# Optimization experiments

Measured on AMD Instinct MI355X. Metric: run time of the kernel, lower is better.

## Reference

```python
import jax, jax.numpy as jnp
import numpy as np

D_MODEL = 1024
NUM_HEADS = 16
D_FF = 4096
MAX_SEQ_LEN = 2048
THETA = 10000.0
EPS = 1e-5
B, S = 2, 2048


def setup_inputs() -> dict:
    key = jax.random.key(0)
    ks = jax.random.split(key, 10)
    scale = 0.02
    inp = {
        "in_features": jax.random.normal(ks[0], (B, S, D_MODEL), dtype=jnp.float32),
        "token_positions": jnp.broadcast_to(jnp.arange(S, dtype=jnp.int32), (B, S)),
        "q_w": jax.random.normal(ks[1], (D_MODEL, D_MODEL), dtype=jnp.float32) * scale,
        "k_w": jax.random.normal(ks[2], (D_MODEL, D_MODEL), dtype=jnp.float32) * scale,
        "v_w": jax.random.normal(ks[3], (D_MODEL, D_MODEL), dtype=jnp.float32) * scale,
        "o_w": jax.random.normal(ks[4], (D_MODEL, D_MODEL), dtype=jnp.float32) * scale,
        "ln1_w": jnp.ones((D_MODEL,), dtype=jnp.float32),
        "ln2_w": jnp.ones((D_MODEL,), dtype=jnp.float32),
        "ffn_w1": jax.random.normal(ks[5], (D_FF, D_MODEL), dtype=jnp.float32) * scale,
        "ffn_w2": jax.random.normal(ks[6], (D_MODEL, D_FF), dtype=jnp.float32) * scale,
        "ffn_w3": jax.random.normal(ks[7], (D_FF, D_MODEL), dtype=jnp.float32) * scale,
    }
    return inp


def _rmsnorm(x, w, eps=EPS):
    return x * jax.lax.rsqrt(jnp.mean(x * x, axis=-1, keepdims=True) + eps) * w


def _rope(x, pos, theta=THETA):
    # x: [B, H, S, Dh]; pos: [B, S] int
    dh = x.shape[-1]
    inv_freq = theta ** (-jnp.arange(0, dh, 2, dtype=jnp.float32) / dh)  # [Dh/2]
    ang = pos.astype(jnp.float32)[..., None] * inv_freq                  # [B, S, Dh/2]
    cos = jnp.cos(ang)[:, None, :, :]  # [B, 1, S, Dh/2]
    sin = jnp.sin(ang)[:, None, :, :]
    x1, x2 = x[..., 0::2], x[..., 1::2]
    r1 = x1 * cos - x2 * sin
    r2 = x1 * sin + x2 * cos
    return jnp.stack([r1, r2], axis=-1).reshape(x.shape)


def _block(x, pos, q_w, k_w, v_w, o_w, ln1_w, ln2_w, w1, w2, w3):
    b, s, d = x.shape
    h, dh = NUM_HEADS, d // NUM_HEADS
    # Pre-LN attention
    xn = _rmsnorm(x, ln1_w)
    q = jnp.einsum('bsd,ed->bse', xn, q_w).reshape(b, s, h, dh).transpose(0, 2, 1, 3)
    k = jnp.einsum('bsd,ed->bse', xn, k_w).reshape(b, s, h, dh).transpose(0, 2, 1, 3)
    v = jnp.einsum('bsd,ed->bse', xn, v_w).reshape(b, s, h, dh).transpose(0, 2, 1, 3)
    q = _rope(q, pos)
    k = _rope(k, pos)
    scores = jnp.einsum('bhqd,bhkd->bhqk', q, k) / jnp.sqrt(jnp.float32(dh))
    causal = jnp.tril(jnp.ones((s, s), dtype=bool))
    scores = jnp.where(causal, scores, jnp.float32(-1e9))
    attn = jax.nn.softmax(scores, axis=-1)
    ctx = jnp.einsum('bhqk,bhkd->bhqd', attn, v).transpose(0, 2, 1, 3).reshape(b, s, d)
    attn_out = jnp.einsum('bsd,ed->bse', ctx, o_w)
    x = x + attn_out
    # Pre-LN SwiGLU FFN
    xn2 = _rmsnorm(x, ln2_w)
    g = jnp.einsum('bsd,fd->bsf', xn2, w1)
    u = jnp.einsum('bsd,fd->bsf', xn2, w3)
    ffn_out = jnp.einsum('bsf,df->bsd', jax.nn.silu(g) * u, w2)
    return x + ffn_out


def reference(in_features, token_positions, q_w, k_w, v_w, o_w, ln1_w, ln2_w, ffn_w1, ffn_w2, ffn_w3):
    return _block(in_features, token_positions, q_w, k_w, v_w, o_w, ln1_w, ln2_w, ffn_w1, ffn_w2, ffn_w3)
```

## Files before the change

kernel.cpp:

```cpp
#include <hip/hip_runtime.h>
#include <hip/hip_bf16.h>

typedef __attribute__((ext_vector_type(8))) __bf16 bf16x8;
typedef __attribute__((ext_vector_type(4))) float f32x4;

#define DEV static __device__ __forceinline__

DEV unsigned short f2bf(float f) {
  __bf16 h = (__bf16)f;
  union { __bf16 h; unsigned short u; } v; v.h = h;
  return v.u;
}
DEV float bf2f(unsigned short h) {
  union { unsigned int u; float f; } v; v.u = ((unsigned int)h) << 16;
  return v.f;
}
DEV unsigned pkbf(float lo, float hi) {
  union { __bf16 h[2]; unsigned u; } v;
  v.h[0] = (__bf16)lo; v.h[1] = (__bf16)hi;
  return v.u;
}
DEV f32x4 mfma16(bf16x8 a, bf16x8 b, f32x4 c) {
  return __builtin_amdgcn_mfma_f32_16x16x32_bf16(a, b, c, 0, 0, 0);
}
DEV void gload_lds16(const void* g, void* l) {
  __builtin_amdgcn_global_load_lds((__attribute__((address_space(1))) void*)g,
                                   (__attribute__((address_space(3))) void*)l,
                                   16, 0, 0);
}
DEV float fexp2(float x) { return exp2f(x); }

struct CvtArgs { const float* src[7]; int cum[8]; };
__global__ __launch_bounds__(256) void cvt_all(CvtArgs a, unsigned short* __restrict__ dst) {
  int i = (blockIdx.x * 256 + threadIdx.x) * 4;
  if (i >= a.cum[7]) return;
  int w = 0;
#pragma unroll 7
  for (int t = 0; t < 7; ++t) if (i >= a.cum[t + 1]) w = t + 1;
  int local = i - a.cum[w];
  int di;
  if (w == 5)      di = 8388608 + ((local >> 10) << 11) + (local & 1023);
  else if (w == 6) di = 8388608 + ((local >> 10) << 11) + 1024 + (local & 1023);
  else             di = i;
  float4 v = *(const float4*)(a.src[w] + local);
  dst[di + 0] = f2bf(v.x);
  dst[di + 1] = f2bf(v.y);
  dst[di + 2] = f2bf(v.z);
  dst[di + 3] = f2bf(v.w);
}

__global__ __launch_bounds__(256) void rmsnorm_k(const float* __restrict__ x,
                                                 const float* __restrict__ w,
                                                 unsigned short* __restrict__ out) {
  int row = blockIdx.x;
  int tid = threadIdx.x;
  const float* xr = x + (size_t)row * 1024;
  float4 v = *(const float4*)(xr + tid * 4);
  float ss = v.x * v.x + v.y * v.y + v.z * v.z + v.w * v.w;
#pragma unroll
  for (int m = 32; m >= 1; m >>= 1) ss += __shfl_xor(ss, m);
  __shared__ float red[4];
  int wid = tid >> 6;
  if ((tid & 63) == 0) red[wid] = ss;
  __syncthreads();
  float tot = red[0] + red[1] + red[2] + red[3];
  float rs = rsqrtf(tot * (1.0f / 1024.0f) + 1e-5f);
  float4 wv = *(const float4*)(w + tid * 4);
  unsigned short* o = out + (size_t)row * 1024 + tid * 4;
  o[0] = f2bf(v.x * rs * wv.x);
  o[1] = f2bf(v.y * rs * wv.y);
  o[2] = f2bf(v.z * rs * wv.z);
  o[3] = f2bf(v.w * rs * wv.w);
}

__global__ __launch_bounds__(256) void rope2_k(unsigned short* __restrict__ q,
                                               unsigned short* __restrict__ k,
                                               const int* __restrict__ pos) {
  int idx = blockIdx.x * 256 + threadIdx.x;
  int i = idx & 31;
  int s = (idx >> 5) & 2047;
  int bh = idx >> 16;
  int b = bh >> 4;
  float p = (float)pos[b * 2048 + s];
  float inv = exp2f(-(float)i * 0.4152410118609203f);
  float ang = p * inv;
  float sn = sinf(ang), cs = cosf(ang);
  size_t base = (((size_t)bh * 2048) + s) * 64 + 2 * i;
  float q1 = bf2f(q[base]), q2 = bf2f(q[base + 1]);
  q[base]     = f2bf(q1 * cs - q2 * sn);
  q[base + 1] = f2bf(q1 * sn + q2 * cs);
  float k1 = bf2f(k[base]), k2 = bf2f(k[base + 1]);
  k[base]     = f2bf(k1 * cs - k2 * sn);
  k[base + 1] = f2bf(k1 * sn + k2 * cs);
}

template <int MODE>
DEV void gemm8_body(const unsigned short* __restrict__ A, int lda,
                    const unsigned short* __restrict__ B, int ldb,
                    int bm, int bn, int kbase, int nt,
                    unsigned short* __restrict__ outb, float* __restrict__ outf,
                    const float* __restrict__ resid,
                    unsigned short* As, unsigned short* Bs) {
  const int tid = threadIdx.x;
  const int lane = tid & 63, wid = tid >> 6;
  const int wr = wid >> 2, wc = wid & 3;
  const int m0 = bm * 256, n0 = bn * 256;

  const int r0 = tid >> 2, r1 = 128 + (tid >> 2), cc = tid & 3;
  const int sc0 = (cc ^ ((r0 >> 1) & 3)) * 8;
  const int sc1 = (cc ^ ((r1 >> 1) & 3)) * 8;
  const size_t arow0 = (size_t)(m0 + r0) * lda, arow1 = (size_t)(m0 + r1) * lda;
  const size_t brow0 = (size_t)(n0 + r0) * ldb, brow1 = (size_t)(n0 + r1) * ldb;
  const int du0 = tid * 8, du1 = (512 + tid) * 8;

  auto stA = [&](int t, int kh) {
    unsigned short* d = As + ((((t & 1) << 1) | kh) * 8192);
    const unsigned short* s = A + kbase + t * 64 + kh * 32;
    gload_lds16(s + arow0 + sc0, d + du0);
    gload_lds16(s + arow1 + sc1, d + du1);
  };
  auto stB = [&](int t, int kh) {
    unsigned short* d = Bs + ((((t & 1) << 1) | kh) * 8192);
    const unsigned short* s = B + kbase + t * 64 + kh * 32;
    gload_lds16(s + brow0 + sc0, d + du0);
    gload_lds16(s + brow1 + sc1, d + du1);
  };

  const int fcol = ((lane >> 4) ^ ((lane >> 1) & 3)) * 8;
  const int frow = lane & 15;
  const int abase = (wr * 128 + frow) * 32 + fcol;
  const int bbase = (wc * 64 + frow) * 32 + fcol;

  f32x4 acc[8][4] = {};
  bf16x8 a[4], b[4];

#define LOADA(buf, ks, mh) { const unsigned short* p_ = As + (((buf) << 1) | (ks)) * 8192 + abase + (mh) * 2048; \
  a[0] = *(const bf16x8*)(p_); a[1] = *(const bf16x8*)(p_ + 512); \
  a[2] = *(const bf16x8*)(p_ + 1024); a[3] = *(const bf16x8*)(p_ + 1536); }
#define LOADB(buf, ks) { const unsigned short* p_ = Bs + (((buf) << 1) | (ks)) * 8192 + bbase; \
  b[0] = *(const bf16x8*)(p_); b[1] = *(const bf16x8*)(p_ + 512); \
  b[2] = *(const bf16x8*)(p_ + 1024); b[3] = *(const bf16x8*)(p_ + 1536); }
#define MFMAQ(mh) { _Pragma("unroll") for (int fi = 0; fi < 4; ++fi) \
  _Pragma("unroll") for (int j = 0; j < 4; ++j) \
    acc[(mh) * 4 + fi][j] = mfma16(a[fi], b[j], acc[(mh) * 4 + fi][j]); }
#define LGK0() { asm volatile("s_waitcnt lgkmcnt(0)" ::: "memory"); }

  stA(0, 0); stB(0, 0); stA(0, 1); stB(0, 1);
  stA(1, 0); stB(1, 0);
  asm volatile("s_waitcnt vmcnt(4)" ::: "memory");
  __builtin_amdgcn_s_barrier();

  for (int t = 0; t < nt; ++t) {
    const int buf = t & 1;
    LOADA(buf, 0, 0); LOADB(buf, 0);
    if (t + 1 < nt) stA(t + 1, 1);
    __builtin_amdgcn_s_barrier();
    LGK0();
    __builtin_amdgcn_s_setprio(1); MFMAQ(0); __builtin_amdgcn_s_setprio(0);
    __builtin_amdgcn_s_barrier();
    LOADA(buf, 0, 1);
    if (t + 1 < nt) stB(t + 1, 1);
    __builtin_amdgcn_s_barrier();
    LGK0();
    __builtin_amdgcn_s_setprio(1); MFMAQ(1); __builtin_amdgcn_s_setprio(0);
    __builtin_amdgcn_s_barrier();
    LOADA(buf, 1, 0); LOADB(buf, 1);
    if (t + 2 < nt) stA(t + 2, 0);
    __builtin_amdgcn_s_barrier();
    LGK0();
    __builtin_amdgcn_s_setprio(1); MFMAQ(0); __builtin_amdgcn_s_setprio(0);
    __builtin_amdgcn_s_barrier();
    LOADA(buf, 1, 1);
    if (t + 2 < nt) stB(t + 2, 0);
    __builtin_amdgcn_s_barrier();
    LGK0();
    __builtin_amdgcn_s_setprio(1); MFMAQ(1); __builtin_amdgcn_s_setprio(0);
    if (t + 1 < nt) {
      if (t + 2 < nt) { asm volatile("s_waitcnt vmcnt(4)" ::: "memory"); }
      else            { asm volatile("s_waitcnt vmcnt(0)" ::: "memory"); }
      __builtin_amdgcn_s_barrier();
    }
  }
#undef LOADA
#undef LOADB
#undef MFMAQ
#undef LGK0

#pragma unroll
  for (int i = 0; i < 8; ++i)
#pragma unroll
    for (int j = 0; j < 4; ++j)
#pragma unroll
      for (int r = 0; r < 4; ++r) {
        int m = m0 + wr * 128 + i * 16 + ((lane >> 4) << 2) + r;
        int n = n0 + wc * 64 + j * 16 + (lane & 15);
        float v = acc[i][j][r];
        if (MODE == 0) {
          unsigned short* dst = outb + ((n >= 1024) ? 4194304 : 0);
          int nn = n & 1023;
          int bb = m >> 11, s = m & 2047, hh = nn >> 6, dd = nn & 63;
          dst[(((size_t)bb * 16 + hh) * 2048 + s) * 64 + dd] = f2bf(v);
        } else if (MODE == 1) {
          int hh = m >> 6, dd = m & 63, bb = n >> 11, s = n & 2047;
          outb[(((size_t)bb * 16 + hh) * 64 + dd) * 2048 + s] = f2bf(v);
        } else if (MODE == 2) {
          size_t idx = (size_t)m * 1024 + n;
          outf[idx] = resid[idx] + v;
        } else if (MODE == 5) {
          outb[(size_t)m * 1024 + n] = f2bf(v);
        } else {
          float other = __shfl_xor(v, 1);
          if (!(lane & 1)) {
            float hv = v / (1.0f + __expf(-v)) * other;
            outb[(size_t)m * 4096 + (n >> 1)] = f2bf(hv);
          }
        }
      }
}

DEV void swz_map(int bid, int nwg, int MT, int& bm, int& bn) {
  int cpx = nwg >> 3;
  int sw = (bid & 7) * cpx + (bid >> 3);
  bm = sw % MT;
  bn = sw / MT;
}

template <int MODE>
__global__ __launch_bounds__(512, 2) void gemm8_k(const unsigned short* __restrict__ A, int lda,
                                                  const unsigned short* __restrict__ B, int ldb,
                                                  int MT, int kz, int nt,
                                                  unsigned short* __restrict__ outb,
                                                  float* __restrict__ outf,
                                                  const float* __restrict__ resid) {
  __shared__ __align__(16) unsigned short lds[65536];
  int bm, bn;
  swz_map(blockIdx.x, gridDim.x, MT, bm, bn);
  int kb = kz * blockIdx.y;
  unsigned short* ob = outb;
  if (MODE == 5) ob += (size_t)blockIdx.y * 4194304;
  gemm8_body<MODE>(A, lda, B, ldb, bm, bn, kb, nt, ob, outf, resid, lds, lds + 32768);
}

__global__ __launch_bounds__(512, 2) void gemm8_qkv(const unsigned short* __restrict__ xn,
                                                    const unsigned short* __restrict__ wqk,
                                                    const unsigned short* __restrict__ wv,
                                                    unsigned short* __restrict__ qk_out,
                                                    unsigned short* __restrict__ vt_out) {
  __shared__ __align__(16) unsigned short lds[65536];
  int bid = blockIdx.x;
  if (bid < 128) {
    int bm, bn;
    swz_map(bid, 128, 16, bm, bn);
    gemm8_body<0>(xn, 1024, wqk, 1024, bm, bn, 0, 16, qk_out, nullptr, nullptr, lds, lds + 32768);
  } else {
    bid -= 128;
    int bm, bn;
    swz_map(bid, 64, 4, bm, bn);
    gemm8_body<1>(wv, 1024, xn, 1024, bm, bn, 0, 16, vt_out, nullptr, nullptr, lds, lds + 32768);
  }
}

template <int K>
__global__ __launch_bounds__(256) void gemm_res(const unsigned short* __restrict__ A,
                                                const unsigned short* __restrict__ Bw,
                                                float* __restrict__ outf,
                                                const float* __restrict__ resid) {
  __shared__ __align__(16) unsigned short As[128 * 64];
  __shared__ __align__(16) unsigned short Bs[128 * 64];
  const int N = 1024;
  const int tid = threadIdx.x;
  const int wid = tid >> 6, lane = tid & 63;
  const int wr = wid >> 1, wc = wid & 1;
  const int m0 = blockIdx.x * 128, n0 = blockIdx.y * 128;
  const int sw = (lane & 7) * 8;
  f32x4 acc[4][4] = {};

  for (int k0 = 0; k0 < K; k0 += 64) {
    __syncthreads();
#pragma unroll
    for (int it = 0; it < 4; ++it) {
      int c = wid * 4 + it;
      int row = c * 8 + (lane >> 3);
      int col = ((lane & 7) ^ (row & 7)) * 8;
      gload_lds16(A + (size_t)(m0 + row) * K + k0 + col, As + c * 512);
      gload_lds16(Bw + (size_t)(n0 + row) * K + k0 + col, Bs + c * 512);
    }
    asm volatile("s_waitcnt vmcnt(0)" ::: "memory");
    __syncthreads();
#pragma unroll
    for (int kk = 0; kk < 2; ++kk) {
      const int kof = (kk * 32 + (lane >> 4) * 8) ^ sw;
      bf16x8 af[4], bfr[4];
#pragma unroll
      for (int i = 0; i < 4; ++i) {
        af[i]  = *(const bf16x8*)(As + (wr * 64 + i * 16 + (lane & 15)) * 64 + kof);
        bfr[i] = *(const bf16x8*)(Bs + (wc * 64 + i * 16 + (lane & 15)) * 64 + kof);
      }
#pragma unroll
      for (int i = 0; i < 4; ++i)
#pragma unroll
        for (int j = 0; j < 4; ++j) acc[i][j] = mfma16(af[i], bfr[j], acc[i][j]);
    }
  }
  const int rb = m0 + wr * 64 + ((lane >> 4) * 4);
  const int cb = n0 + wc * 64 + (lane & 15);
#pragma unroll
  for (int i = 0; i < 4; ++i)
#pragma unroll
    for (int r = 0; r < 4; ++r) {
      int m = rb + i * 16 + r;
#pragma unroll
      for (int j = 0; j < 4; ++j) {
        size_t idx = (size_t)m * N + cb + j * 16;
        outf[idx] = resid[idx] + acc[i][j][r];
      }
    }
}

__global__ __launch_bounds__(256) void reduce_k(float* __restrict__ out,
                                                const unsigned short* __restrict__ partb) {
  int i = (blockIdx.x * 256 + threadIdx.x) * 4;
  float4 o = *(const float4*)(out + i);
#pragma unroll
  for (int s = 0; s < 4; ++s) {
    uint2 w = *(const uint2*)(partb + (size_t)s * 4194304 + i);
    o.x += bf2f((unsigned short)(w.x & 0xffff));
    o.y += bf2f((unsigned short)(w.x >> 16));
    o.z += bf2f((unsigned short)(w.y & 0xffff));
    o.w += bf2f((unsigned short)(w.y >> 16));
  }
  *(float4*)(out + i) = o;
}

__global__ __launch_bounds__(256) void attn_k(const unsigned short* __restrict__ q,
                                              const unsigned short* __restrict__ k,
                                              const unsigned short* __restrict__ vt,
                                              unsigned short* __restrict__ ctx) {
  __shared__ __align__(16) unsigned short Ks[2][4096];
  __shared__ __align__(16) unsigned short Vs[2][4096];
  __shared__ __align__(16) unsigned short Ps[4][16 * 72];
  const int bid = blockIdx.x;
  const int bh = (bid & 7) * 4 + ((bid >> 3) & 3);
  const int qt = 31 - (bid >> 5);
  const int tid = threadIdx.x, wid = tid >> 6, lane = tid & 63;
  const size_t bhS = (size_t)bh * 2048;
  const size_t bhD = (size_t)bh * 64 * 2048;
  const int b = bh >> 4, hh = bh & 15;
  const int sw = (lane & 7) * 8;
  const int h4 = lane >> 4, l15 = lane & 15;
  const float SC2 = 0.18033688011112042f;

  const int c0 = wid * 2, c1 = wid * 2 + 1;
  const int row0 = c0 * 8 + (lane >> 3), row1 = c1 * 8 + (lane >> 3);
  const int col0 = ((lane & 7) ^ (row0 & 7)) * 8;
  const int col1 = ((lane & 7) ^ (row1 & 7)) * 8;

  auto stage = [&](int kt, int buf) {
    gload_lds16(k + (bhS + kt * 64 + row0) * 64 + col0, &Ks[buf][c0 * 512]);
    gload_lds16(k + (bhS + kt * 64 + row1) * 64 + col1, &Ks[buf][c1 * 512]);
    gload_lds16(vt + bhD + (size_t)row0 * 2048 + kt * 64 + col0, &Vs[buf][c0 * 512]);
    gload_lds16(vt + bhD + (size_t)row1 * 2048 + kt * 64 + col1, &Vs[buf][c1 * 512]);
  };

  const int q0 = qt * 64;
  bf16x8 qf[2];
  {
    const unsigned short* qp = q + (bhS + q0 + wid * 16 + l15) * 64 + h4 * 8;
    qf[0] = *(const bf16x8*)qp;
    qf[1] = *(const bf16x8*)(qp + 32);
#pragma unroll
    for (int jj = 0; jj < 8; ++jj) {
      qf[0][jj] = (__bf16)((float)qf[0][jj] * SC2);
      qf[1][jj] = (__bf16)((float)qf[1][jj] * SC2);
    }
  }
  float mrow = -1e30f, lrow = 0.0f;
  f32x4 o[4] = {};
  const int qg = q0 + wid * 16 + l15;
  const int rowb = q0 + wid * 16 + (h4 << 2);

  stage(0, 0);
  if (qt > 0) { stage(1, 1); asm volatile("s_waitcnt vmcnt(4)" ::: "memory"); }
  else        {              asm volatile("s_waitcnt vmcnt(0)" ::: "memory"); }
  __builtin_amdgcn_s_barrier();

  for (int kt = 0; kt <= qt; ++kt) {
    const int cur = kt & 1;
    float s[16];
#pragma unroll
    for (int nt = 0; nt < 4; ++nt) {
      f32x4 z = {};
#pragma unroll
      for (int ks = 0; ks < 2; ++ks) {
        int kof = (ks * 32 + h4 * 8) ^ sw;
        bf16x8 kf = *(const bf16x8*)(&Ks[cur][(nt * 16 + l15) * 64 + kof]);
        z = mfma16(kf, qf[ks], z);
      }
      s[nt * 4 + 0] = z[0]; s[nt * 4 + 1] = z[1];
      s[nt * 4 + 2] = z[2]; s[nt * 4 + 3] = z[3];
    }
    if (kt == qt) {
#pragma unroll
      for (int nt = 0; nt < 4; ++nt)
#pragma unroll
        for (int r = 0; r < 4; ++r) {
          int key = q0 + nt * 16 + (h4 << 2) + r;
          if (key > qg) s[nt * 4 + r] = -3e38f;
        }
    }
    float pmax = s[0];
#pragma unroll
    for (int i = 1; i < 16; ++i) pmax = fmaxf(pmax, s[i]);
    pmax = fmaxf(pmax, __shfl_xor(pmax, 16));
    pmax = fmaxf(pmax, __shfl_xor(pmax, 32));
    if (!__all(pmax <= mrow + 11.5f)) {
      float mnew = fmaxf(mrow, pmax);
      float dl = mrow - mnew;
      mrow = mnew;
      lrow *= fexp2(dl);
#pragma unroll
      for (int r = 0; r < 4; ++r) {
        float ar = fexp2(__shfl(dl, (h4 << 2) + r, 16));
#pragma unroll
        for (int d = 0; d < 4; ++d) o[d][r] *= ar;
      }
    }
    float sum = 0.0f;
#pragma unroll
    for (int i = 0; i < 16; ++i) { s[i] = fexp2(s[i] - mrow); sum += s[i]; }
    lrow += sum;
    {
      unsigned short* pr = &Ps[wid][l15 * 72 + (h4 << 2)];
#pragma unroll
      for (int nt = 0; nt < 4; ++nt) {
        uint2 w;
        w.x = pkbf(s[4 * nt], s[4 * nt + 1]);
        w.y = pkbf(s[4 * nt + 2], s[4 * nt + 3]);
        *(uint2*)(pr + nt * 16) = w;
      }
    }
#pragma unroll
    for (int ks = 0; ks < 2; ++ks) {
      bf16x8 pf = *(const bf16x8*)(&Ps[wid][l15 * 72 + ks * 32 + (h4 << 3)]);
      int kof = (ks * 32 + h4 * 8) ^ sw;
#pragma unroll
      for (int d = 0; d < 4; ++d) {
        bf16x8 vf = *(const bf16x8*)(&Vs[cur][(d * 16 + l15) * 64 + kof]);
        o[d] = mfma16(pf, vf, o[d]);
      }
    }
    __builtin_amdgcn_s_barrier();
    if (kt + 2 <= qt) {
      stage(kt + 2, cur);
      asm volatile("s_waitcnt vmcnt(4)" ::: "memory");
    } else if (kt + 1 <= qt) {
      asm volatile("s_waitcnt vmcnt(0)" ::: "memory");
    }
    __builtin_amdgcn_s_barrier();
  }
  lrow += __shfl_xor(lrow, 16);
  lrow += __shfl_xor(lrow, 32);
  float inv = 1.0f / lrow;
#pragma unroll
  for (int r = 0; r < 4; ++r) {
    float invr = __shfl(inv, (h4 << 2) + r, 16);
#pragma unroll
    for (int d = 0; d < 4; ++d)
      ctx[((size_t)b * 2048 + (rowb + r)) * 1024 + hh * 64 + d * 16 + l15] = f2bf(o[d][r] * invr);
  }
}

extern "C" void kernel_launch(void* const* d_in, const int* in_sizes, int n_in,
                              void* d_out, int out_size, void* d_ws, size_t ws_size,
                              hipStream_t stream) {
  (void)in_sizes; (void)n_in; (void)out_size; (void)ws_size;
  const float* in_f = (const float*)d_in[0];
  const int* pos    = (const int*)d_in[1];
  const float* q_w  = (const float*)d_in[2];
  const float* k_w  = (const float*)d_in[3];
  const float* v_w  = (const float*)d_in[4];
  const float* o_w  = (const float*)d_in[5];
  const float* ln1  = (const float*)d_in[6];
  const float* ln2  = (const float*)d_in[7];
  const float* w1   = (const float*)d_in[8];
  const float* w2   = (const float*)d_in[9];
  const float* w3   = (const float*)d_in[10];
  float* out = (float*)d_out;

  unsigned short* ws = (unsigned short*)d_ws;
  unsigned short* wb   = ws;
  unsigned short* wqkb = wb;
  unsigned short* wvb  = wb + 2097152;
  unsigned short* wob  = wb + 3145728;
  unsigned short* w2b  = wb + 4194304;
  unsigned short* w13b = wb + 8388608;
  unsigned short* xn   = ws + 16777216;
  unsigned short* qb   = ws + 20971520;
  unsigned short* kb   = ws + 25165824;
  unsigned short* vb   = ws + 29360128;
  unsigned short* cx   = ws + 33554432;
  unsigned short* partb = ws + 20971520;
  unsigned short* hb   = ws + 54525952;

  CvtArgs ca;
  ca.src[0] = q_w; ca.src[1] = k_w; ca.src[2] = v_w; ca.src[3] = o_w;
  ca.src[4] = w2;  ca.src[5] = w1;  ca.src[6] = w3;
  ca.cum[0] = 0;        ca.cum[1] = 1048576;  ca.cum[2] = 2097152;  ca.cum[3] = 3145728;
  ca.cum[4] = 4194304;  ca.cum[5] = 8388608;  ca.cum[6] = 12582912; ca.cum[7] = 16777216;
  cvt_all<<<16384, 256, 0, stream>>>(ca, wb);

  rmsnorm_k<<<4096, 256, 0, stream>>>(in_f, ln1, xn);

  gemm8_qkv<<<192, 512, 0, stream>>>(xn, wqkb, wvb, qb, vb);

  rope2_k<<<8192, 256, 0, stream>>>(qb, kb, pos);

  attn_k<<<1024, 256, 0, stream>>>(qb, kb, vb, cx);

  gemm_res<1024><<<dim3(32, 8), 256, 0, stream>>>(cx, wob, out, in_f);

  rmsnorm_k<<<4096, 256, 0, stream>>>(out, ln2, xn);

  gemm8_k<6><<<512, 512, 0, stream>>>(xn, 1024, w13b, 1024, 16, 0, 16, hb, nullptr, nullptr);

  gemm8_k<5><<<dim3(64, 4), 512, 0, stream>>>(hb, 4096, w2b, 4096, 16, 1024, 16, partb, nullptr, nullptr);

  reduce_k<<<4096, 256, 0, stream>>>(out, partb);
}
```

Baseline: 281.9 us.

## Switch 256x256 GEMMs from 8 waves to 4 waves with 128x128 per wave

The block-tiled bf16 MFMA GEMM used for QKV and both FFN projections now runs 256 threads instead of 512. Each wave computes a 128x128 sub-tile (8x8 accumulator fragments) instead of 128x64. This doubles the reuse of each LDS fragment load per MFMA and halves barrier participants. Each thread now issues four global-to-LDS loads per stage instead of two. The trade-off is heavy register pressure from 256 accumulator registers and fewer resident waves to hide latency. The unused residual epilogue mode is also dropped.

```diff
diff --git a/kernel.cpp b/kernel.cpp
--- a/kernel.cpp
+++ b/kernel.cpp
@@ -95,105 +95,105 @@
 }
 
 template <int MODE>
-DEV void gemm8_body(const unsigned short* __restrict__ A, int lda,
+DEV void gemm4_body(const unsigned short* __restrict__ A, int lda,
                     const unsigned short* __restrict__ B, int ldb,
                     int bm, int bn, int kbase, int nt,
-                    unsigned short* __restrict__ outb, float* __restrict__ outf,
-                    const float* __restrict__ resid,
+                    unsigned short* __restrict__ outb,
                     unsigned short* As, unsigned short* Bs) {
   const int tid = threadIdx.x;
   const int lane = tid & 63, wid = tid >> 6;
-  const int wr = wid >> 2, wc = wid & 3;
+  const int wr = wid >> 1, wc = wid & 1;
   const int m0 = bm * 256, n0 = bn * 256;
 
-  const int r0 = tid >> 2, r1 = 128 + (tid >> 2), cc = tid & 3;
-  const int sc0 = (cc ^ ((r0 >> 1) & 3)) * 8;
-  const int sc1 = (cc ^ ((r1 >> 1) & 3)) * 8;
-  const size_t arow0 = (size_t)(m0 + r0) * lda, arow1 = (size_t)(m0 + r1) * lda;
-  const size_t brow0 = (size_t)(n0 + r0) * ldb, brow1 = (size_t)(n0 + r1) * ldb;
-  const int du0 = tid * 8, du1 = (512 + tid) * 8;
+  const int r0 = tid >> 2, cc = tid & 3;
+  const int sc = (cc ^ ((r0 >> 1) & 3)) * 8;
+  const int du = tid * 8;
 
   auto stA = [&](int t, int kh) {
     unsigned short* d = As + ((((t & 1) << 1) | kh) * 8192);
-    const unsigned short* s = A + kbase + t * 64 + kh * 32;
-    gload_lds16(s + arow0 + sc0, d + du0);
-    gload_lds16(s + arow1 + sc1, d + du1);
+    const unsigned short* s = A + kbase + t * 64 + kh * 32 + sc;
+#pragma unroll
+    for (int uu = 0; uu < 4; ++uu)
+      gload_lds16(s + (size_t)(m0 + r0 + 64 * uu) * lda, d + du + uu * 2048);
   };
   auto stB = [&](int t, int kh) {
     unsigned short* d = Bs + ((((t & 1) << 1) | kh) * 8192);
-    const unsigned short* s = B + kbase + t * 64 + kh * 32;
-    gload_lds16(s + brow0 + sc0, d + du0);
-    gload_lds16(s + brow1 + sc1, d + du1);
+    const unsigned short* s = B + kbase + t * 64 + kh * 32 + sc;
+#pragma unroll
+    for (int uu = 0; uu < 4; ++uu)
+      gload_lds16(s + (size_t)(n0 + r0 + 64 * uu) * ldb, d + du + uu * 2048);
   };
 
   const int fcol = ((lane >> 4) ^ ((lane >> 1) & 3)) * 8;
   const int frow = lane & 15;
   const int abase = (wr * 128 + frow) * 32 + fcol;
-  const int bbase = (wc * 64 + frow) * 32 + fcol;
-
-  f32x4 acc[8][4] = {};
-  bf16x8 a[4], b[4];
-
-#define LOADA(buf, ks, mh) { const unsigned short* p_ = As + (((buf) << 1) | (ks)) * 8192 + abase + (mh) * 2048; \
-  a[0] = *(const bf16x8*)(p_); a[1] = *(const bf16x8*)(p_ + 512); \
+  const int bbase = (wc * 128 + frow) * 32 + fcol;
+
+  f32x4 acc[8][8] = {};
+  bf16x8 a[4], b[8];
+
+#define LOADA4(buf, ks, mh) { const unsigned short* p_ = As + (((buf) << 1) | (ks)) * 8192 + abase + (mh) * 2048; \
+  a[0] = *(const bf16x8*)(p_);        a[1] = *(const bf16x8*)(p_ + 512); \
   a[2] = *(const bf16x8*)(p_ + 1024); a[3] = *(const bf16x8*)(p_ + 1536); }
-#define LOADB(buf, ks) { const unsigned short* p_ = Bs + (((buf) << 1) | (ks)) * 8192 + bbase; \
-  b[0] = *(const bf16x8*)(p_); b[1] = *(const bf16x8*)(p_ + 512); \
-  b[2] = *(const bf16x8*)(p_ + 1024); b[3] = *(const bf16x8*)(p_ + 1536); }
-#define MFMAQ(mh) { _Pragma("unroll") for (int fi = 0; fi < 4; ++fi) \
-  _Pragma("unroll") for (int j = 0; j < 4; ++j) \
+#define LOADB4(buf, ks) { const unsigned short* p_ = Bs + (((buf) << 1) | (ks)) * 8192 + bbase; \
+  b[0] = *(const bf16x8*)(p_);        b[1] = *(const bf16x8*)(p_ + 512); \
+  b[2] = *(const bf16x8*)(p_ + 1024); b[3] = *(const bf16x8*)(p_ + 1536); \
+  b[4] = *(const bf16x8*)(p_ + 2048); b[5] = *(const bf16x8*)(p_ + 2560); \
+  b[6] = *(const bf16x8*)(p_ + 3072); b[7] = *(const bf16x8*)(p_ + 3584); }
+#define MFMAQ4(mh) { _Pragma("unroll") for (int fi = 0; fi < 4; ++fi) \
+  _Pragma("unroll") for (int j = 0; j < 8; ++j) \
     acc[(mh) * 4 + fi][j] = mfma16(a[fi], b[j], acc[(mh) * 4 + fi][j]); }
 #define LGK0() { asm volatile("s_waitcnt lgkmcnt(0)" ::: "memory"); }
 
   stA(0, 0); stB(0, 0); stA(0, 1); stB(0, 1);
   stA(1, 0); stB(1, 0);
-  asm volatile("s_waitcnt vmcnt(4)" ::: "memory");
+  asm volatile("s_waitcnt vmcnt(8)" ::: "memory");
   __builtin_amdgcn_s_barrier();
 
   for (int t = 0; t < nt; ++t) {
     const int buf = t & 1;
-    LOADA(buf, 0, 0); LOADB(buf, 0);
+    LOADA4(buf, 0, 0); LOADB4(buf, 0);
     if (t + 1 < nt) stA(t + 1, 1);
     __builtin_amdgcn_s_barrier();
     LGK0();
-    __builtin_amdgcn_s_setprio(1); MFMAQ(0); __builtin_amdgcn_s_setprio(0);
-    __builtin_amdgcn_s_barrier();
-    LOADA(buf, 0, 1);
+    __builtin_amdgcn_s_setprio(1); MFMAQ4(0); __builtin_amdgcn_s_setprio(0);
+    __builtin_amdgcn_s_barrier();
+    LOADA4(buf, 0, 1);
     if (t + 1 < nt) stB(t + 1, 1);
     __builtin_amdgcn_s_barrier();
     LGK0();
-    __builtin_amdgcn_s_setprio(1); MFMAQ(1); __builtin_amdgcn_s_setprio(0);
-    __builtin_amdgcn_s_barrier();
-    LOADA(buf, 1, 0); LOADB(buf, 1);
+    __builtin_amdgcn_s_setprio(1); MFMAQ4(1); __builtin_amdgcn_s_setprio(0);
+    __builtin_amdgcn_s_barrier();
+    LOADA4(buf, 1, 0); LOADB4(buf, 1);
     if (t + 2 < nt) stA(t + 2, 0);
     __builtin_amdgcn_s_barrier();
     LGK0();
-    __builtin_amdgcn_s_setprio(1); MFMAQ(0); __builtin_amdgcn_s_setprio(0);
-    __builtin_amdgcn_s_barrier();
-    LOADA(buf, 1, 1);
+    __builtin_amdgcn_s_setprio(1); MFMAQ4(0); __builtin_amdgcn_s_setprio(0);
+    __builtin_amdgcn_s_barrier();
+    LOADA4(buf, 1, 1);
     if (t + 2 < nt) stB(t + 2, 0);
     __builtin_amdgcn_s_barrier();
     LGK0();
-    __builtin_amdgcn_s_setprio(1); MFMAQ(1); __builtin_amdgcn_s_setprio(0);
+    __builtin_amdgcn_s_setprio(1); MFMAQ4(1); __builtin_amdgcn_s_setprio(0);
     if (t + 1 < nt) {
-      if (t + 2 < nt) { asm volatile("s_waitcnt vmcnt(4)" ::: "memory"); }
+      if (t + 2 < nt) { asm volatile("s_waitcnt vmcnt(8)" ::: "memory"); }
       else            { asm volatile("s_waitcnt vmcnt(0)" ::: "memory"); }
       __builtin_amdgcn_s_barrier();
     }
   }
-#undef LOADA
-#undef LOADB
-#undef MFMAQ
+#undef LOADA4
+#undef LOADB4
+#undef MFMAQ4
 #undef LGK0
 
 #pragma unroll
   for (int i = 0; i < 8; ++i)
 #pragma unroll
-    for (int j = 0; j < 4; ++j)
+    for (int j = 0; j < 8; ++j)
 #pragma unroll
       for (int r = 0; r < 4; ++r) {
-        int m = m0 + wr * 128 + i * 16 + ((lane >> 4) << 2) + r;
-        int n = n0 + wc * 64 + j * 16 + (lane & 15);
+        int m = m0 + wr * 128 + (i >> 2) * 64 + (i & 3) * 16 + ((lane >> 4) << 2) + r;
+        int n = n0 + wc * 128 + j * 16 + (lane & 15);
         float v = acc[i][j][r];
         if (MODE == 0) {
           unsigned short* dst = outb + ((n >= 1024) ? 4194304 : 0);
@@ -203,9 +203,6 @@
         } else if (MODE == 1) {
           int hh = m >> 6, dd = m & 63, bb = n >> 11, s = n & 2047;
           outb[(((size_t)bb * 16 + hh) * 64 + dd) * 2048 + s] = f2bf(v);
-        } else if (MODE == 2) {
-          size_t idx = (size_t)m * 1024 + n;
-          outf[idx] = resid[idx] + v;
         } else if (MODE == 5) {
           outb[(size_t)m * 1024 + n] = f2bf(v);
         } else {
@@ -226,22 +223,20 @@
 }
 
 template <int MODE>
-__global__ __launch_bounds__(512, 2) void gemm8_k(const unsigned short* __restrict__ A, int lda,
+__global__ __launch_bounds__(256, 1) void gemm4_k(const unsigned short* __restrict__ A, int lda,
                                                   const unsigned short* __restrict__ B, int ldb,
                                                   int MT, int kz, int nt,
-                                                  unsigned short* __restrict__ outb,
-                                                  float* __restrict__ outf,
-                                                  const float* __restrict__ resid) {
+                                                  unsigned short* __restrict__ outb) {
   __shared__ __align__(16) unsigned short lds[65536];
   int bm, bn;
   swz_map(blockIdx.x, gridDim.x, MT, bm, bn);
   int kb = kz * blockIdx.y;
   unsigned short* ob = outb;
   if (MODE == 5) ob += (size_t)blockIdx.y * 4194304;
-  gemm8_body<MODE>(A, lda, B, ldb, bm, bn, kb, nt, ob, outf, resid, lds, lds + 32768);
-}
-
-__global__ __launch_bounds__(512, 2) void gemm8_qkv(const unsigned short* __restrict__ xn,
+  gemm4_body<MODE>(A, lda, B, ldb, bm, bn, kb, nt, ob, lds, lds + 32768);
+}
+
+__global__ __launch_bounds__(256, 1) void gemm4_qkv(const unsigned short* __restrict__ xn,
                                                     const unsigned short* __restrict__ wqk,
                                                     const unsigned short* __restrict__ wv,
                                                     unsigned short* __restrict__ qk_out,
@@ -251,12 +246,12 @@
   if (bid < 128) {
     int bm, bn;
     swz_map(bid, 128, 16, bm, bn);
-    gemm8_body<0>(xn, 1024, wqk, 1024, bm, bn, 0, 16, qk_out, nullptr, nullptr, lds, lds + 32768);
+    gemm4_body<0>(xn, 1024, wqk, 1024, bm, bn, 0, 16, qk_out, lds, lds + 32768);
   } else {
     bid -= 128;
     int bm, bn;
     swz_map(bid, 64, 4, bm, bn);
-    gemm8_body<1>(wv, 1024, xn, 1024, bm, bn, 0, 16, vt_out, nullptr, nullptr, lds, lds + 32768);
+    gemm4_body<1>(wv, 1024, xn, 1024, bm, bn, 0, 16, vt_out, lds, lds + 32768);
   }
 }
 
@@ -511,7 +506,7 @@
 
   rmsnorm_k<<<4096, 256, 0, stream>>>(in_f, ln1, xn);
 
-  gemm8_qkv<<<192, 512, 0, stream>>>(xn, wqkb, wvb, qb, vb);
+  gemm4_qkv<<<192, 256, 0, stream>>>(xn, wqkb, wvb, qb, vb);
 
   rope2_k<<<8192, 256, 0, stream>>>(qb, kb, pos);
 
@@ -521,9 +516,9 @@
 
   rmsnorm_k<<<4096, 256, 0, stream>>>(out, ln2, xn);
 
-  gemm8_k<6><<<512, 512, 0, stream>>>(xn, 1024, w13b, 1024, 16, 0, 16, hb, nullptr, nullptr);
-
-  gemm8_k<5><<<dim3(64, 4), 512, 0, stream>>>(hb, 4096, w2b, 4096, 16, 1024, 16, partb, nullptr, nullptr);
+  gemm4_k<6><<<512, 256, 0, stream>>>(xn, 1024, w13b, 1024, 16, 0, 16, hb);
+
+  gemm4_k<5><<<dim3(64, 4), 256, 0, stream>>>(hb, 4096, w2b, 4096, 16, 1024, 16, partb);
 
   reduce_k<<<4096, 256, 0, stream>>>(out, partb);
 }
```

After: 344.7 us. 22.3% more time.

## Replace 256x256 pipelined GEMMs with simpler 128x128 single-buffer GEMM kernel

Applied to the files above, without the earlier changes.

Removes the 256x256-tile, 512-thread, double-buffered GEMM body with fine-grained barrier/prio scheduling. All projection GEMMs (QKV, FFN up, FFN down split-K) now use the simpler 128x128 tile, 256-thread kernel already used for the output projection, with more blocks per launch. This raises block count and occupancy, but loses the load/compute overlap and the larger per-tile reuse, and adds global traffic.

```diff
diff --git a/kernel.cpp b/kernel.cpp
--- a/kernel.cpp
+++ b/kernel.cpp
@@ -95,105 +95,57 @@
 }
 
 template <int MODE>
-DEV void gemm8_body(const unsigned short* __restrict__ A, int lda,
+DEV void gemm2_body(const unsigned short* __restrict__ A, int lda,
                     const unsigned short* __restrict__ B, int ldb,
-                    int bm, int bn, int kbase, int nt,
+                    int m0, int n0, int kbase, int nk,
                     unsigned short* __restrict__ outb, float* __restrict__ outf,
                     const float* __restrict__ resid,
                     unsigned short* As, unsigned short* Bs) {
   const int tid = threadIdx.x;
-  const int lane = tid & 63, wid = tid >> 6;
-  const int wr = wid >> 2, wc = wid & 3;
-  const int m0 = bm * 256, n0 = bn * 256;
-
-  const int r0 = tid >> 2, r1 = 128 + (tid >> 2), cc = tid & 3;
-  const int sc0 = (cc ^ ((r0 >> 1) & 3)) * 8;
-  const int sc1 = (cc ^ ((r1 >> 1) & 3)) * 8;
-  const size_t arow0 = (size_t)(m0 + r0) * lda, arow1 = (size_t)(m0 + r1) * lda;
-  const size_t brow0 = (size_t)(n0 + r0) * ldb, brow1 = (size_t)(n0 + r1) * ldb;
-  const int du0 = tid * 8, du1 = (512 + tid) * 8;
-
-  auto stA = [&](int t, int kh) {
-    unsigned short* d = As + ((((t & 1) << 1) | kh) * 8192);
-    const unsigned short* s = A + kbase + t * 64 + kh * 32;
-    gload_lds16(s + arow0 + sc0, d + du0);
-    gload_lds16(s + arow1 + sc1, d + du1);
-  };
-  auto stB = [&](int t, int kh) {
-    unsigned short* d = Bs + ((((t & 1) << 1) | kh) * 8192);
-    const unsigned short* s = B + kbase + t * 64 + kh * 32;
-    gload_lds16(s + brow0 + sc0, d + du0);
-    gload_lds16(s + brow1 + sc1, d + du1);
-  };
-
-  const int fcol = ((lane >> 4) ^ ((lane >> 1) & 3)) * 8;
-  const int frow = lane & 15;
-  const int abase = (wr * 128 + frow) * 32 + fcol;
-  const int bbase = (wc * 64 + frow) * 32 + fcol;
-
-  f32x4 acc[8][4] = {};
-  bf16x8 a[4], b[4];
-
-#define LOADA(buf, ks, mh) { const unsigned short* p_ = As + (((buf) << 1) | (ks)) * 8192 + abase + (mh) * 2048; \
-  a[0] = *(const bf16x8*)(p_); a[1] = *(const bf16x8*)(p_ + 512); \
-  a[2] = *(const bf16x8*)(p_ + 1024); a[3] = *(const bf16x8*)(p_ + 1536); }
-#define LOADB(buf, ks) { const unsigned short* p_ = Bs + (((buf) << 1) | (ks)) * 8192 + bbase; \
-  b[0] = *(const bf16x8*)(p_); b[1] = *(const bf16x8*)(p_ + 512); \
-  b[2] = *(const bf16x8*)(p_ + 1024); b[3] = *(const bf16x8*)(p_ + 1536); }
-#define MFMAQ(mh) { _Pragma("unroll") for (int fi = 0; fi < 4; ++fi) \
-  _Pragma("unroll") for (int j = 0; j < 4; ++j) \
-    acc[(mh) * 4 + fi][j] = mfma16(a[fi], b[j], acc[(mh) * 4 + fi][j]); }
-#define LGK0() { asm volatile("s_waitcnt lgkmcnt(0)" ::: "memory"); }
-
-  stA(0, 0); stB(0, 0); stA(0, 1); stB(0, 1);
-  stA(1, 0); stB(1, 0);
-  asm volatile("s_waitcnt vmcnt(4)" ::: "memory");
-  __builtin_amdgcn_s_barrier();
-
-  for (int t = 0; t < nt; ++t) {
-    const int buf = t & 1;
-    LOADA(buf, 0, 0); LOADB(buf, 0);
-    if (t + 1 < nt) stA(t + 1, 1);
-    __builtin_amdgcn_s_barrier();
-    LGK0();
-    __builtin_amdgcn_s_setprio(1); MFMAQ(0); __builtin_amdgcn_s_setprio(0);
-    __builtin_amdgcn_s_barrier();
-    LOADA(buf, 0, 1);
-    if (t + 1 < nt) stB(t + 1, 1);
-    __builtin_amdgcn_s_barrier();
-    LGK0();
-    __builtin_amdgcn_s_setprio(1); MFMAQ(1); __builtin_amdgcn_s_setprio(0);
-    __builtin_amdgcn_s_barrier();
-    LOADA(buf, 1, 0); LOADB(buf, 1);
-    if (t + 2 < nt) stA(t + 2, 0);
-    __builtin_amdgcn_s_barrier();
-    LGK0();
-    __builtin_amdgcn_s_setprio(1); MFMAQ(0); __builtin_amdgcn_s_setprio(0);
-    __builtin_amdgcn_s_barrier();
-    LOADA(buf, 1, 1);
-    if (t + 2 < nt) stB(t + 2, 0);
-    __builtin_amdgcn_s_barrier();
-    LGK0();
-    __builtin_amdgcn_s_setprio(1); MFMAQ(1); __builtin_amdgcn_s_setprio(0);
-    if (t + 1 < nt) {
-      if (t + 2 < nt) { asm volatile("s_waitcnt vmcnt(4)" ::: "memory"); }
-      else            { asm volatile("s_waitcnt vmcnt(0)" ::: "memory"); }
-      __builtin_amdgcn_s_barrier();
-    }
-  }
-#undef LOADA
-#undef LOADB
-#undef MFMAQ
-#undef LGK0
-
-#pragma unroll
-  for (int i = 0; i < 8; ++i)
-#pragma unroll
-    for (int j = 0; j < 4; ++j)
-#pragma unroll
-      for (int r = 0; r < 4; ++r) {
-        int m = m0 + wr * 128 + i * 16 + ((lane >> 4) << 2) + r;
-        int n = n0 + wc * 64 + j * 16 + (lane & 15);
+  const int wid = tid >> 6, lane = tid & 63;
+  const int wr = wid >> 1, wc = wid & 1;
+  const int sw = (lane & 7) * 8;
+  f32x4 acc[4][4] = {};
+
+  for (int t = 0; t < nk; ++t) {
+    int k0 = kbase + t * 64;
+    __syncthreads();
+#pragma unroll
+    for (int it = 0; it < 4; ++it) {
+      int c = wid * 4 + it;
+      int row = c * 8 + (lane >> 3);
+      int col = ((lane & 7) ^ (row & 7)) * 8;
+      gload_lds16(A + (size_t)(m0 + row) * lda + k0 + col, As + c * 512);
+      gload_lds16(B + (size_t)(n0 + row) * ldb + k0 + col, Bs + c * 512);
+    }
+    asm volatile("s_waitcnt vmcnt(0)" ::: "memory");
+    __syncthreads();
+#pragma unroll
+    for (int kk = 0; kk < 2; ++kk) {
+      const int kof = (kk * 32 + (lane >> 4) * 8) ^ sw;
+      bf16x8 af[4], bfr[4];
+#pragma unroll
+      for (int i = 0; i < 4; ++i) {
+        af[i]  = *(const bf16x8*)(As + (wr * 64 + i * 16 + (lane & 15)) * 64 + kof);
+        bfr[i] = *(const bf16x8*)(Bs + (wc * 64 + i * 16 + (lane & 15)) * 64 + kof);
+      }
+#pragma unroll
+      for (int i = 0; i < 4; ++i)
+#pragma unroll
+        for (int j = 0; j < 4; ++j) acc[i][j] = mfma16(af[i], bfr[j], acc[i][j]);
+    }
+  }
+
+  const int rb = m0 + wr * 64 + ((lane >> 4) * 4);
+  const int cb = n0 + wc * 64 + (lane & 15);
+#pragma unroll
+  for (int i = 0; i < 4; ++i)
+#pragma unroll
+    for (int r = 0; r < 4; ++r) {
+      int m = rb + i * 16 + r;
+#pragma unroll
+      for (int j = 0; j < 4; ++j) {
+        int n = cb + j * 16;
         float v = acc[i][j][r];
         if (MODE == 0) {
           unsigned short* dst = outb + ((n >= 1024) ? 4194304 : 0);
@@ -216,105 +168,41 @@
           }
         }
       }
-}
-
-DEV void swz_map(int bid, int nwg, int MT, int& bm, int& bn) {
-  int cpx = nwg >> 3;
-  int sw = (bid & 7) * cpx + (bid >> 3);
-  bm = sw % MT;
-  bn = sw / MT;
+    }
 }
 
 template <int MODE>
-__global__ __launch_bounds__(512, 2) void gemm8_k(const unsigned short* __restrict__ A, int lda,
-                                                  const unsigned short* __restrict__ B, int ldb,
-                                                  int MT, int kz, int nt,
-                                                  unsigned short* __restrict__ outb,
-                                                  float* __restrict__ outf,
-                                                  const float* __restrict__ resid) {
-  __shared__ __align__(16) unsigned short lds[65536];
-  int bm, bn;
-  swz_map(blockIdx.x, gridDim.x, MT, bm, bn);
-  int kb = kz * blockIdx.y;
-  unsigned short* ob = outb;
-  if (MODE == 5) ob += (size_t)blockIdx.y * 4194304;
-  gemm8_body<MODE>(A, lda, B, ldb, bm, bn, kb, nt, ob, outf, resid, lds, lds + 32768);
-}
-
-__global__ __launch_bounds__(512, 2) void gemm8_qkv(const unsigned short* __restrict__ xn,
-                                                    const unsigned short* __restrict__ wqk,
-                                                    const unsigned short* __restrict__ wv,
-                                                    unsigned short* __restrict__ qk_out,
-                                                    unsigned short* __restrict__ vt_out) {
-  __shared__ __align__(16) unsigned short lds[65536];
-  int bid = blockIdx.x;
-  if (bid < 128) {
-    int bm, bn;
-    swz_map(bid, 128, 16, bm, bn);
-    gemm8_body<0>(xn, 1024, wqk, 1024, bm, bn, 0, 16, qk_out, nullptr, nullptr, lds, lds + 32768);
-  } else {
-    bid -= 128;
-    int bm, bn;
-    swz_map(bid, 64, 4, bm, bn);
-    gemm8_body<1>(wv, 1024, xn, 1024, bm, bn, 0, 16, vt_out, nullptr, nullptr, lds, lds + 32768);
-  }
-}
-
-template <int K>
-__global__ __launch_bounds__(256) void gemm_res(const unsigned short* __restrict__ A,
-                                                const unsigned short* __restrict__ Bw,
-                                                float* __restrict__ outf,
-                                                const float* __restrict__ resid) {
+__global__ __launch_bounds__(256) void gemm2_k(const unsigned short* __restrict__ A, int lda,
+                                               const unsigned short* __restrict__ B, int ldb,
+                                               int nk,
+                                               unsigned short* __restrict__ outb,
+                                               float* __restrict__ outf,
+                                               const float* __restrict__ resid) {
   __shared__ __align__(16) unsigned short As[128 * 64];
   __shared__ __align__(16) unsigned short Bs[128 * 64];
-  const int N = 1024;
-  const int tid = threadIdx.x;
-  const int wid = tid >> 6, lane = tid & 63;
-  const int wr = wid >> 1, wc = wid & 1;
-  const int m0 = blockIdx.x * 128, n0 = blockIdx.y * 128;
-  const int sw = (lane & 7) * 8;
-  f32x4 acc[4][4] = {};
-
-  for (int k0 = 0; k0 < K; k0 += 64) {
-    __syncthreads();
-#pragma unroll
-    for (int it = 0; it < 4; ++it) {
-      int c = wid * 4 + it;
-      int row = c * 8 + (lane >> 3);
-      int col = ((lane & 7) ^ (row & 7)) * 8;
-      gload_lds16(A + (size_t)(m0 + row) * K + k0 + col, As + c * 512);
-      gload_lds16(Bw + (size_t)(n0 + row) * K + k0 + col, Bs + c * 512);
-    }
-    asm volatile("s_waitcnt vmcnt(0)" ::: "memory");
-    __syncthreads();
-#pragma unroll
-    for (int kk = 0; kk < 2; ++kk) {
-      const int kof = (kk * 32 + (lane >> 4) * 8) ^ sw;
-      bf16x8 af[4], bfr[4];
-#pragma unroll
-      for (int i = 0; i < 4; ++i) {
-        af[i]  = *(const bf16x8*)(As + (wr * 64 + i * 16 + (lane & 15)) * 64 + kof);
-        bfr[i] = *(const bf16x8*)(Bs + (wc * 64 + i * 16 + (lane & 15)) * 64 + kof);
-      }
-#pragma unroll
-      for (int i = 0; i < 4; ++i)
-#pragma unroll
-        for (int j = 0; j < 4; ++j) acc[i][j] = mfma16(af[i], bfr[j], acc[i][j]);
-    }
-  }
-  const int rb = m0 + wr * 64 + ((lane >> 4) * 4);
-  const int cb = n0 + wc * 64 + (lane & 15);
-#pragma unroll
-  for (int i = 0; i < 4; ++i)
-#pragma unroll
-    for (int r = 0; r < 4; ++r) {
-      int m = rb + i * 16 + r;
-#pragma unroll
-      for (int j = 0; j < 4; ++j) {
-        size_t idx = (size_t)m * N + cb + j * 16;
-        outf[idx] = resid[idx] + acc[i][j][r];
-      }
-    }
+  int m0 = blockIdx.x * 128, n0 = blockIdx.y * 128;
+  int kbase = 0;
+  unsigned short* ob = outb;
+  if (MODE == 5) { kbase = blockIdx.z * 1024; ob += (size_t)blockIdx.z * 4194304; }
+  gemm2_body<MODE>(A, lda, B, ldb, m0, n0, kbase, nk, ob, outf, resid, As, Bs);
+}
+
+__global__ __launch_bounds__(256) void gemm2_qkv(const unsigned short* __restrict__ xn,
+                                                 const unsigned short* __restrict__ wqk,
+                                                 const unsigned short* __restrict__ wv,
+                                                 unsigned short* __restrict__ qk_out,
+                                                 unsigned short* __restrict__ vt_out) {
+  __shared__ __align__(16) unsigned short As[128 * 64];
+  __shared__ __align__(16) unsigned short Bs[128 * 64];
+  int bid = blockIdx.x;
+  if (bid < 512) {
+    int m0 = (bid & 31) * 128, n0 = (bid >> 5) * 128;
+    gemm2_body<0>(xn, 1024, wqk, 1024, m0, n0, 0, 16, qk_out, nullptr, nullptr, As, Bs);
+  } else {
+    bid -= 512;
+    int m0 = (bid & 7) * 128, n0 = (bid >> 3) * 128;
+    gemm2_body<1>(wv, 1024, xn, 1024, m0, n0, 0, 16, vt_out, nullptr, nullptr, As, Bs);
+  }
 }
 
 __global__ __launch_bounds__(256) void reduce_k(float* __restrict__ out,
@@ -511,19 +399,19 @@
 
   rmsnorm_k<<<4096, 256, 0, stream>>>(in_f, ln1, xn);
 
-  gemm8_qkv<<<192, 512, 0, stream>>>(xn, wqkb, wvb, qb, vb);
+  gemm2_qkv<<<768, 256, 0, stream>>>(xn, wqkb, wvb, qb, vb);
 
   rope2_k<<<8192, 256, 0, stream>>>(qb, kb, pos);
 
   attn_k<<<1024, 256, 0, stream>>>(qb, kb, vb, cx);
 
-  gemm_res<1024><<<dim3(32, 8), 256, 0, stream>>>(cx, wob, out, in_f);
+  gemm2_k<2><<<dim3(32, 8), 256, 0, stream>>>(cx, 1024, wob, 1024, 16, nullptr, out, in_f);
 
   rmsnorm_k<<<4096, 256, 0, stream>>>(out, ln2, xn);
 
-  gemm8_k<6><<<512, 512, 0, stream>>>(xn, 1024, w13b, 1024, 16, 0, 16, hb, nullptr, nullptr);
-
-  gemm8_k<5><<<dim3(64, 4), 512, 0, stream>>>(hb, 4096, w2b, 4096, 16, 1024, 16, partb, nullptr, nullptr);
+  gemm2_k<6><<<dim3(32, 64), 256, 0, stream>>>(xn, 1024, w13b, 1024, 16, hb, nullptr, nullptr);
+
+  gemm2_k<5><<<dim3(32, 8, 4), 256, 0, stream>>>(hb, 4096, w2b, 4096, 16, partb, nullptr, nullptr);
 
   reduce_k<<<4096, 256, 0, stream>>>(out, partb);
 }
```

After: 301.4 us. 6.9% more time.
